# Performance work log

Hardware: AMD Instinct MI355X
Metric: run time of the kernel (lower is better)

Reference implementation:

```python
import jax, jax.numpy as jnp
import numpy as np

B, D, DEPTH, C = 8192, 2048, 10, 1000
NUM_INNER = 2 ** DEPTH - 1   # 1023
NUM_LEAVES = 2 ** DEPTH      # 1024


def setup_inputs() -> dict:
    key = jax.random.key(0)
    k1, k2, k3, k4 = jax.random.split(key, 4)
    x = jax.random.normal(k1, (B, D), dtype=jnp.float32)
    # scale weights like a typical init so sigmoid isn't fully saturated
    W = jax.random.normal(k2, (D, NUM_INNER), dtype=jnp.float32) * 0.02
    b = jax.random.normal(k3, (NUM_INNER,), dtype=jnp.float32) * 0.02
    leaf_dist = jax.random.normal(k4, (NUM_LEAVES, C), dtype=jnp.float32)
    return {"x": x, "W": W, "b": b, "leaf_dist": leaf_dist}


def reference(x, W, b, leaf_dist):
    # inner node routing probabilities: [B, num_inner]
    decisions = jax.nn.sigmoid(x @ W + b)
    depth = int(np.log2(decisions.shape[1] + 1))
    pp = jnp.ones((x.shape[0], 1), dtype=x.dtype)  # path probs, starts at root
    for d in range(depth):  # small fixed loop over tree depth
        s, e = 2 ** d - 1, 2 ** (d + 1) - 1
        ld = decisions[:, s:e]                      # [B, 2^d]
        pp = jnp.concatenate([pp * ld, pp * (1.0 - ld)], axis=1)  # [B, 2^(d+1)]
        # faithful reproduction of the original's even/odd reordering
        pp = jnp.concatenate([pp[:, ::2], pp[:, 1::2]], axis=1)
    leaf_probs = jax.nn.softmax(leaf_dist, axis=1)  # [num_leaves, C]
    return pp @ leaf_probs                          # [B, C]
```

## Files before the change

kernel.cpp:

```cpp
#include <hip/hip_runtime.h>

typedef __attribute__((ext_vector_type(8))) unsigned short ushort8v;
typedef __attribute__((ext_vector_type(8))) __bf16 bf16x8;
typedef __attribute__((ext_vector_type(4))) float floatx4;

__device__ __forceinline__ unsigned short f2b(float f) {
    unsigned u = __float_as_uint(f);
    unsigned r = u + 0x7fffu + ((u >> 16) & 1u);
    return (unsigned short)(r >> 16);
}
__device__ __forceinline__ float b2f(unsigned short h) {
    return __uint_as_float(((unsigned)h) << 16);
}

__device__ __forceinline__ void gload16(const unsigned short* g, unsigned short* l) {
    __builtin_amdgcn_global_load_lds(
        (const __attribute__((address_space(1))) unsigned int*)g,
        (__attribute__((address_space(3))) unsigned int*)l,
        16, 0, 0);
}


__global__ __launch_bounds__(256) void prep_kernel(const float* __restrict__ x,
                                                   unsigned short* __restrict__ A2x,
                                                   const float* __restrict__ W,
                                                   unsigned short* __restrict__ B2w,
                                                   const float* __restrict__ ld_,
                                                   unsigned short* __restrict__ B2p) {
    __shared__ float tile[32 * 33];
    __shared__ float buf[1000];
    __shared__ float red[8];
    const int b = blockIdx.x, t = threadIdx.x;
    if (b < 2048) {
        const int mt = b >> 2, kq = (b & 3) * 64;
        const int kco = t >> 4, l16 = t & 15;
        const float* xr0 = x + (size_t)(mt * 16 + l16) * 2048;
#pragma unroll
        for (int i = 0; i < 4; i++) {
            const int kc = kq + i * 16 + kco;
            const float* xr = xr0 + kc * 8;
            float4 v0 = *(const float4*)xr;
            float4 v1 = *(const float4*)(xr + 4);
            ushort8v o;
            o[0] = f2b(v0.x); o[1] = f2b(v0.y); o[2] = f2b(v0.z); o[3] = f2b(v0.w);
            o[4] = f2b(v1.x); o[5] = f2b(v1.y); o[6] = f2b(v1.z); o[7] = f2b(v1.w);
            *(ushort8v*)(A2x + ((size_t)(mt * 256 + kc) * 16 + l16) * 8) = o;
        }
    } else if (b < 4096) {
        const int idx = b - 2048;
        const int n0 = (idx & 31) * 32, k0 = (idx >> 5) * 32;
        const int tx = t & 31, ty = t >> 5;
#pragma unroll
        for (int i = 0; i < 4; i++) {
            int k = k0 + ty + i * 8, n = n0 + tx;
            tile[(ty + i * 8) * 33 + tx] = (n < 1023) ? W[(size_t)k * 1023 + n] : 0.f;
        }
        __syncthreads();
#pragma unroll
        for (int i = 0; i < 4; i++) {
            int n = n0 + ty + i * 8, k = k0 + tx;
            size_t off = ((size_t)((n >> 4) * 256 + (k >> 3)) * 16 + (n & 15)) * 8 + (k & 7);
            B2w[off] = f2b(tile[tx * 33 + ty + i * 8]);
        }
    } else {
        const int l0 = b - 4096;
        const float* r = ld_ + (size_t)l0 * 1000;
        float mx = -3.4e38f;
        for (int i = t; i < 1000; i += 256) { float v = r[i]; buf[i] = v; mx = fmaxf(mx, v); }
#pragma unroll
        for (int o = 32; o > 0; o >>= 1) mx = fmaxf(mx, __shfl_down(mx, o));
        if ((t & 63) == 0) red[t >> 6] = mx;
        __syncthreads();
        mx = fmaxf(fmaxf(red[0], red[1]), fmaxf(red[2], red[3]));
        float s = 0.f;
        for (int i = t; i < 1000; i += 256) { float e = __expf(buf[i] - mx); buf[i] = e; s += e; }
#pragma unroll
        for (int o = 32; o > 0; o >>= 1) s += __shfl_down(s, o);
        if ((t & 63) == 0) red[4 + (t >> 6)] = s;
        __syncthreads();
        float inv = 1.f / (red[4] + red[5] + red[6] + red[7]);
        for (int i = t; i < 1024; i += 256) {
            float pv = (i < 1000) ? buf[i] * inv : 0.f;
            size_t off = ((size_t)((i >> 4) * 128 + (l0 >> 3)) * 16 + (i & 15)) * 8 + (l0 & 7);
            B2p[off] = f2b(pv);
        }
    }
}

__global__ __launch_bounds__(256) void pp_kernel(const unsigned short* __restrict__ dec,
                                                 unsigned short* __restrict__ A2p) {
    __shared__ unsigned short dsh[8 * 1024];
    __shared__ float pa[8 * 1024];
    __shared__ float pb[8 * 1024];
    const int t = threadIdx.x;
    const int r0 = blockIdx.x * 8;
    {
        const ushort8v* src = (const ushort8v*)(dec + (size_t)r0 * 1024);
        ushort8v* dst = (ushort8v*)dsh;
        for (int g = t; g < 1024; g += 256) dst[g] = src[g];
    }
    if (t < 8) pa[t * 1024] = 1.f;
    __syncthreads();
    float* cur = pa; float* nxt = pb;
    for (int dep = 0; dep < 10; dep++) {
        const int half = 1 << dep;
        const int len  = half << 1;
        const int total = len << 3;
        for (int idx = t; idx < total; idx += 256) {
            const int r = idx >> (dep + 1);
            const int j = idx & (len - 1);
            int tt = j >> dep;
            int s  = j & (half - 1);
            int i2 = 2 * s + tt;
            int u  = i2 >> dep;
            int rr = i2 & (half - 1);
            float dv = b2f(dsh[r * 1024 + half - 1 + rr]);
            nxt[r * 1024 + j] = cur[r * 1024 + rr] * (u ? (1.f - dv) : dv);
        }
        __syncthreads();
        float* tmp = cur; cur = nxt; nxt = tmp;
    }
    for (int i = t; i < 8192; i += 256) {
        const int r = i >> 10, j = i & 1023;
        const int rrow = r0 + r;
        size_t off = ((size_t)((rrow >> 4) * 128 + (j >> 3)) * 16 + (rrow & 15)) * 8 + (j & 7);
        A2p[off] = f2b(cur[r * 1024 + j]);
    }
}

template <int EPI>
__global__ __launch_bounds__(256, 2) void gemm_lds(const unsigned short* __restrict__ A2,
                                                   const unsigned short* __restrict__ B2,
                                                   const float* __restrict__ bias,
                                                   unsigned short* __restrict__ obf,
                                                   float* __restrict__ of32,
                                                   int KC, int ldo) {
    __shared__ unsigned short ldsA[2][8192];
    __shared__ unsigned short ldsB[2][8192];

    const int tid  = threadIdx.x;
    const int lane = tid & 63;
    const int wave = tid >> 6;
    const int quad = lane >> 4, l16 = lane & 15;
    const int wr = wave >> 1, wc = wave & 1;

    const int l   = blockIdx.x;
    const int xcd = l & 7;
    const int j   = l >> 3;
    const int bm  = xcd * 8 + (j & 7);
    const int bn  = j >> 3;

    const int cBase = tid >> 4;
    const int sub   = (tid & 15) * 8;
    const unsigned short* srcA[4];
    const unsigned short* srcB[4];
#pragma unroll
    for (int i = 0; i < 4; i++) {
        const int c  = i * 16 + cBase;
        const int mi = c >> 3, kcq = c & 7;
        srcA[i] = A2 + ((size_t)(bm * 8 + mi) * KC + kcq) * 128 + sub;
        srcB[i] = B2 + ((size_t)(bn * 8 + mi) * KC + kcq) * 128 + sub;
    }

    floatx4 acc[4][4] = {};
    const int nks = KC >> 3;

#pragma unroll
    for (int i = 0; i < 4; i++) {
        const int c = i * 16 + cBase;
        gload16(srcA[i], &ldsA[0][c * 128 + sub]);
        gload16(srcB[i], &ldsB[0][c * 128 + sub]);
    }
    __syncthreads();

    int buf = 0;
    for (int ks = 0; ks < nks; ks++) {
        if (ks + 1 < nks) {
            const size_t ko = (size_t)(ks + 1) * 1024;
#pragma unroll
            for (int i = 0; i < 4; i++) {
                const int c = i * 16 + cBase;
                gload16(srcA[i] + ko, &ldsA[buf ^ 1][c * 128 + sub]);
                gload16(srcB[i] + ko, &ldsB[buf ^ 1][c * 128 + sub]);
            }
        }
#pragma unroll
        for (int kk = 0; kk < 2; kk++) {
            bf16x8 af[4], bfv[4];
#pragma unroll
            for (int m2 = 0; m2 < 4; m2++)
                af[m2] = __builtin_bit_cast(bf16x8,
                    *(const ushort8v*)&ldsA[buf][((wr * 4 + m2) * 8 + kk * 4 + quad) * 128 + l16 * 8]);
#pragma unroll
            for (int n2 = 0; n2 < 4; n2++)
                bfv[n2] = __builtin_bit_cast(bf16x8,
                    *(const ushort8v*)&ldsB[buf][((wc * 4 + n2) * 8 + kk * 4 + quad) * 128 + l16 * 8]);
#pragma unroll
            for (int m2 = 0; m2 < 4; m2++)
#pragma unroll
                for (int n2 = 0; n2 < 4; n2++)
                    acc[m2][n2] = __builtin_amdgcn_mfma_f32_16x16x32_bf16(
                        af[m2], bfv[n2], acc[m2][n2], 0, 0, 0);
        }
        __syncthreads();
        buf ^= 1;
    }

    const int mt0 = bm * 8 + wr * 4;
    const int nt0 = bn * 8 + wc * 4;
#pragma unroll
    for (int n2 = 0; n2 < 4; n2++) {
        const int col = (nt0 + n2) * 16 + l16;
        float bb = 0.f;
        if constexpr (EPI == 0) bb = (col < 1023) ? bias[col] : 0.f;
#pragma unroll
        for (int m2 = 0; m2 < 4; m2++) {
            const int row0 = (mt0 + m2) * 16 + quad * 4;
#pragma unroll
            for (int r = 0; r < 4; r++) {
                float v = acc[m2][n2][r];
                if constexpr (EPI == 0) {
                    float sgm = 1.f / (1.f + __expf(-(v + bb)));
                    obf[(size_t)(row0 + r) * ldo + col] = f2b(sgm);
                } else {
                    if (col < 1000) of32[(size_t)(row0 + r) * ldo + col] = v;
                }
            }
        }
    }
}

extern "C" void kernel_launch(void* const* d_in, const int* in_sizes, int n_in,
                              void* d_out, int out_size, void* d_ws, size_t ws_size,
                              hipStream_t stream) {
    const float* x   = (const float*)d_in[0];
    const float* W   = (const float*)d_in[1];
    const float* b   = (const float*)d_in[2];
    const float* ldd = (const float*)d_in[3];
    float* out = (float*)d_out;

    char* ws = (char*)d_ws;
    unsigned short* A2x = (unsigned short*)(ws);
    unsigned short* A2p = (unsigned short*)(ws);
    unsigned short* B2w = (unsigned short*)(ws + 33554432);
    unsigned short* dec = (unsigned short*)(ws + 37748736);
    unsigned short* B2p = (unsigned short*)(ws + 54525952);

    prep_kernel<<<5120, 256, 0, stream>>>(x, A2x, W, B2w, ldd, B2p);
    gemm_lds<0><<<512, 256, 0, stream>>>(A2x, B2w, b, dec, nullptr, 256, 1024);
    pp_kernel<<<1024, 256, 0, stream>>>(dec, A2p);
    gemm_lds<1><<<512, 256, 0, stream>>>(A2p, B2p, nullptr, nullptr, out, 128, 1000);
}
```

Before: 202.6 us.

## Replace double-buffered GEMM with 5-stage pipelined 256x128 tile kernel

Both GEMMs move to a new kernel with 512 threads per block and 256x128 output tiles, where each of the eight waves computes a 64x64 sub-tile. K-chunks are smaller and go through a 5-deep LDS ring buffer filled by direct global-to-LDS loads, with explicit vmcnt waits, barriers and raised MFMA priority. The goal is to hide global-load latency better and get more reuse per block. The cost is 120KB of LDS per block, which limits occupancy, plus hand-written waitcnt logic that depends on exact load counts.

```diff
diff --git a/kernel.cpp b/kernel.cpp
--- a/kernel.cpp
+++ b/kernel.cpp
@@ -128,15 +128,46 @@
     }
 }
 
-template <int EPI>
-__global__ __launch_bounds__(256, 2) void gemm_lds(const unsigned short* __restrict__ A2,
-                                                   const unsigned short* __restrict__ B2,
-                                                   const float* __restrict__ bias,
-                                                   unsigned short* __restrict__ obf,
-                                                   float* __restrict__ of32,
-                                                   int KC, int ldo) {
-    __shared__ unsigned short ldsA[2][8192];
-    __shared__ unsigned short ldsB[2][8192];
+#define VMW(N) asm volatile("s_waitcnt vmcnt(" #N ")" ::: "memory")
+
+#define P5_STEP(ks_, b_, VM_, DOSTAGE_)                                           \
+    {                                                                             \
+        VMW(VM_);                                                                 \
+        __builtin_amdgcn_s_barrier();                                             \
+        __builtin_amdgcn_sched_barrier(0);                                        \
+        const unsigned short* lA = &lds[(b_)][0];                                 \
+        const unsigned short* lB = &lds[(b_)][8192];                              \
+        bf16x8 af[4], bv[4];                                                      \
+        _Pragma("unroll")                                                         \
+        for (int m2 = 0; m2 < 4; m2++)                                            \
+            af[m2] = __builtin_bit_cast(bf16x8,                                   \
+                *(const ushort8v*)&lA[(wr * 4 + m2) * 512 + quad * 128 + l16 * 8]); \
+        _Pragma("unroll")                                                         \
+        for (int n2 = 0; n2 < 4; n2++)                                            \
+            bv[n2] = __builtin_bit_cast(bf16x8,                                   \
+                *(const ushort8v*)&lB[(wc * 4 + n2) * 512 + quad * 128 + l16 * 8]); \
+        asm volatile("s_waitcnt lgkmcnt(0)" ::: "memory");                        \
+        __builtin_amdgcn_sched_barrier(0);                                        \
+        __builtin_amdgcn_s_barrier();                                             \
+        __builtin_amdgcn_sched_barrier(0);                                        \
+        if (DOSTAGE_) STAGE((ks_) + 5, (b_));                                     \
+        __builtin_amdgcn_s_setprio(1);                                            \
+        _Pragma("unroll")                                                         \
+        for (int m2 = 0; m2 < 4; m2++)                                            \
+            _Pragma("unroll")                                                     \
+            for (int n2 = 0; n2 < 4; n2++)                                        \
+                acc[m2][n2] = __builtin_amdgcn_mfma_f32_16x16x32_bf16(            \
+                    af[m2], bv[n2], acc[m2][n2], 0, 0, 0);                        \
+        __builtin_amdgcn_s_setprio(0);                                            \
+    }
+
+template <int EPI, int KC>
+__global__ __launch_bounds__(512, 2) void gemm_p5(const unsigned short* __restrict__ A2,
+                                                  const unsigned short* __restrict__ B2,
+                                                  const float* __restrict__ bias,
+                                                  unsigned short* __restrict__ obf,
+                                                  float* __restrict__ of32, int ldo) {
+    __shared__ unsigned short lds[5][12288];
 
     const int tid  = threadIdx.x;
     const int lane = tid & 63;
@@ -144,75 +175,49 @@
     const int quad = lane >> 4, l16 = lane & 15;
     const int wr = wave >> 1, wc = wave & 1;
 
-    const int l   = blockIdx.x;
-    const int xcd = l & 7;
-    const int j   = l >> 3;
-    const int bm  = xcd * 8 + (j & 7);
-    const int bn  = j >> 3;
-
-    const int cBase = tid >> 4;
-    const int sub   = (tid & 15) * 8;
-    const unsigned short* srcA[4];
-    const unsigned short* srcB[4];
-#pragma unroll
-    for (int i = 0; i < 4; i++) {
-        const int c  = i * 16 + cBase;
-        const int mi = c >> 3, kcq = c & 7;
-        srcA[i] = A2 + ((size_t)(bm * 8 + mi) * KC + kcq) * 128 + sub;
-        srcB[i] = B2 + ((size_t)(bn * 8 + mi) * KC + kcq) * 128 + sub;
-    }
+    const int bid = blockIdx.x;
+    const int xcd = bid & 7;
+    const int j   = bid >> 3;
+    const int bm  = xcd * 4 + (j & 3);
+    const int bn  = j >> 2;
+
+    const unsigned short* gA0 = A2 + ((size_t)(bm * 16 + wave * 2)     * KC + quad) * 128 + l16 * 8;
+    const unsigned short* gA1 = A2 + ((size_t)(bm * 16 + wave * 2 + 1) * KC + quad) * 128 + l16 * 8;
+    const unsigned short* gB0 = B2 + ((size_t)(bn * 8  + wave)         * KC + quad) * 128 + l16 * 8;
+    const int dA0 = (wave * 8 + quad) * 128 + l16 * 8;
+    const int dA1 = dA0 + 512;
+    const int dB0 = 8192 + (wave * 4 + quad) * 128 + l16 * 8;
 
     floatx4 acc[4][4] = {};
-    const int nks = KC >> 3;
-
-#pragma unroll
-    for (int i = 0; i < 4; i++) {
-        const int c = i * 16 + cBase;
-        gload16(srcA[i], &ldsA[0][c * 128 + sub]);
-        gload16(srcB[i], &ldsB[0][c * 128 + sub]);
-    }
-    __syncthreads();
-
-    int buf = 0;
-    for (int ks = 0; ks < nks; ks++) {
-        if (ks + 1 < nks) {
-            const size_t ko = (size_t)(ks + 1) * 1024;
-#pragma unroll
-            for (int i = 0; i < 4; i++) {
-                const int c = i * 16 + cBase;
-                gload16(srcA[i] + ko, &ldsA[buf ^ 1][c * 128 + sub]);
-                gload16(srcB[i] + ko, &ldsB[buf ^ 1][c * 128 + sub]);
-            }
-        }
-#pragma unroll
-        for (int kk = 0; kk < 2; kk++) {
-            bf16x8 af[4], bfv[4];
-#pragma unroll
-            for (int m2 = 0; m2 < 4; m2++)
-                af[m2] = __builtin_bit_cast(bf16x8,
-                    *(const ushort8v*)&ldsA[buf][((wr * 4 + m2) * 8 + kk * 4 + quad) * 128 + l16 * 8]);
-#pragma unroll
-            for (int n2 = 0; n2 < 4; n2++)
-                bfv[n2] = __builtin_bit_cast(bf16x8,
-                    *(const ushort8v*)&ldsB[buf][((wc * 4 + n2) * 8 + kk * 4 + quad) * 128 + l16 * 8]);
-#pragma unroll
-            for (int m2 = 0; m2 < 4; m2++)
-#pragma unroll
-                for (int n2 = 0; n2 < 4; n2++)
-                    acc[m2][n2] = __builtin_amdgcn_mfma_f32_16x16x32_bf16(
-                        af[m2], bfv[n2], acc[m2][n2], 0, 0, 0);
-        }
-        __syncthreads();
-        buf ^= 1;
-    }
-
-    const int mt0 = bm * 8 + wr * 4;
-    const int nt0 = bn * 8 + wc * 4;
+    constexpr int nks = KC / 4;
+
+    auto STAGE = [&](int ks, int b) {
+        const size_t ko = (size_t)ks * 512;
+        gload16(gA0 + ko, &lds[b][dA0]);
+        gload16(gA1 + ko, &lds[b][dA1]);
+        gload16(gB0 + ko, &lds[b][dB0]);
+    };
+
+    STAGE(0, 0); STAGE(1, 1); STAGE(2, 2); STAGE(3, 3); STAGE(4, 4);
+
+    int bb = 0;
+    for (int ks = 0; ks < nks - 5; ++ks) {
+        P5_STEP(ks, bb, 12, true);
+        bb = (bb == 4) ? 0 : bb + 1;
+    }
+    P5_STEP(nks - 5, (nks - 5) % 5, 12, false);
+    P5_STEP(nks - 4, (nks - 4) % 5, 9,  false);
+    P5_STEP(nks - 3, (nks - 3) % 5, 6,  false);
+    P5_STEP(nks - 2, (nks - 2) % 5, 3,  false);
+    P5_STEP(nks - 1, (nks - 1) % 5, 0,  false);
+
+    const int mt0 = bm * 16 + wr * 4;
+    const int nt0 = bn * 8  + wc * 4;
 #pragma unroll
     for (int n2 = 0; n2 < 4; n2++) {
         const int col = (nt0 + n2) * 16 + l16;
-        float bb = 0.f;
-        if constexpr (EPI == 0) bb = (col < 1023) ? bias[col] : 0.f;
+        float bbias = 0.f;
+        if constexpr (EPI == 0) bbias = (col < 1023) ? bias[col] : 0.f;
 #pragma unroll
         for (int m2 = 0; m2 < 4; m2++) {
             const int row0 = (mt0 + m2) * 16 + quad * 4;
@@ -220,7 +225,7 @@
             for (int r = 0; r < 4; r++) {
                 float v = acc[m2][n2][r];
                 if constexpr (EPI == 0) {
-                    float sgm = 1.f / (1.f + __expf(-(v + bb)));
+                    float sgm = 1.f / (1.f + __expf(-(v + bbias)));
                     obf[(size_t)(row0 + r) * ldo + col] = f2b(sgm);
                 } else {
                     if (col < 1000) of32[(size_t)(row0 + r) * ldo + col] = v;
@@ -247,7 +252,7 @@
     unsigned short* B2p = (unsigned short*)(ws + 54525952);
 
     prep_kernel<<<5120, 256, 0, stream>>>(x, A2x, W, B2w, ldd, B2p);
-    gemm_lds<0><<<512, 256, 0, stream>>>(A2x, B2w, b, dec, nullptr, 256, 1024);
+    gemm_p5<0, 256><<<256, 512, 0, stream>>>(A2x, B2w, b, dec, nullptr, 1024);
     pp_kernel<<<1024, 256, 0, stream>>>(dec, A2p);
-    gemm_lds<1><<<512, 256, 0, stream>>>(A2p, B2p, nullptr, nullptr, out, 128, 1000);
-}
+    gemm_p5<1, 128><<<256, 512, 0, stream>>>(A2p, B2p, nullptr, nullptr, out, 1000);
+}
```

Result: slower. 209.1 us (+3.2%).
